# Kernel optimization log

Hardware: AMD Instinct MI355X
Metric: run time of the kernel (lower is better)

## Reference

```python
import jax, jax.numpy as jnp
import numpy as np

SIZE = 11
SIGMA = 1.5
K1, K2, L = 0.01, 0.03, 1.0
C1 = (K1 * L) ** 2
C2 = (K2 * L) ** 2


def _fspecial_gauss(size=SIZE, sigma=SIGMA):
    # mimic MATLAB fspecial('gaussian'): grid -5..5 for size=11
    x, y = np.mgrid[-size // 2 + 1:size // 2 + 1, -size // 2 + 1:size // 2 + 1]
    g = np.exp(-((x.astype(np.float32) ** 2 + y.astype(np.float32) ** 2) / (2.0 * sigma ** 2)))
    g = g / g.sum()
    return jnp.asarray(g, dtype=jnp.float32)[None, None]  # [1,1,11,11] OIHW


def _conv_valid(x, w):
    # x: [B,1,H,W], w: [1,1,k,k], stride 1, no padding
    return jax.lax.conv_general_dilated(
        x, w, window_strides=(1, 1), padding='VALID',
        dimension_numbers=('NCHW', 'OIHW', 'NCHW'))


def setup_inputs() -> dict:
    key = jax.random.key(0)
    k1, k2 = jax.random.split(key)
    sr_image = jax.random.uniform(k1, (16, 3, 512, 512), dtype=jnp.float32)
    hr_image = jax.random.uniform(k2, (16, 3, 512, 512), dtype=jnp.float32)
    return {"sr_image": sr_image, "hr_image": hr_image}


def reference(sr_image, hr_image):
    hr = hr_image[:, 0:1, :, :]
    sr = sr_image[:, 0:1, :, :]
    window = _fspecial_gauss()
    mu1 = _conv_valid(hr, window)
    mu2 = _conv_valid(sr, window)
    mu1_sq = mu1 * mu1
    mu2_sq = mu2 * mu2
    mu1_mu2 = mu1 * mu2
    sigma1_sq = _conv_valid(hr * hr, window) - mu1_sq
    sigma2_sq = _conv_valid(sr * sr, window) - mu2_sq
    sigma12 = _conv_valid(hr * sr, window) - mu1_mu2
    value = ((2 * mu1_mu2 + C1) * (2 * sigma12 + C2)
             / ((mu1_sq + mu2_sq + C1) * (sigma1_sq + sigma2_sq + C2)))
    return jnp.mean(value)
```

## Files before the change

kernel.cpp:

```cpp
#include <hip/hip_runtime.h>
#include <math.h>

#define TW 32
#define TH 32
#define HR 42
#define IMG_W 512
#define OUT_W 502
#define CH_STRIDE (3 * IMG_W * IMG_W)
#define NBLK 4096

__global__ __launch_bounds__(256) void ssim_main_kernel(
    const float* __restrict__ sr_img,
    const float* __restrict__ hr_img,
    float* __restrict__ partial)
{
    __shared__ float hf[5][HR][TW];
    __shared__ float red[4];

    const int t  = threadIdx.x;
    const int x0 = blockIdx.x * TW;
    const int y0 = blockIdx.y * TH;
    const int b  = blockIdx.z;

    float w[11];
    {
        float s = 0.f;
#pragma unroll
        for (int i = 0; i < 11; ++i) {
            float d = (float)(i - 5);
            w[i] = expf(-d * d / 4.5f);
            s += w[i];
        }
        float inv = 1.f / s;
#pragma unroll
        for (int i = 0; i < 11; ++i) w[i] *= inv;
    }

    const float* __restrict__ hrp = hr_img + (size_t)b * CH_STRIDE;
    const float* __restrict__ srp = sr_img + (size_t)b * CH_STRIDE;

    if (t < 168) {
        int r  = t >> 2;
        int c0 = (t & 3) * 8;
        int gy = y0 + r; if (gy > IMG_W - 1) gy = IMG_W - 1;
        const float4* hrow = (const float4*)(hrp + (size_t)gy * IMG_W + x0 + c0);
        const float4* srow = (const float4*)(srp + (size_t)gy * IMG_W + x0 + c0);

        float h[20], s[20];
#pragma unroll
        for (int q = 0; q < 5; ++q) {
            float4 va = hrow[q];
            h[4*q] = va.x; h[4*q+1] = va.y; h[4*q+2] = va.z; h[4*q+3] = va.w;
            float4 vb = srow[q];
            s[4*q] = vb.x; s[4*q+1] = vb.y; s[4*q+2] = vb.z; s[4*q+3] = vb.w;
        }

        float m1[8], m2[8], x2[8], y2[8], xy[8];
#pragma unroll
        for (int j = 0; j < 8; ++j) { m1[j]=0.f; m2[j]=0.f; x2[j]=0.f; y2[j]=0.f; xy[j]=0.f; }
#pragma unroll
        for (int k = 0; k < 11; ++k) {
            float wk = w[k];
#pragma unroll
            for (int j = 0; j < 8; ++j) {
                float a = h[j + k], bb = s[j + k];
                float u = wk * a, v = wk * bb;
                m1[j] += u;      m2[j] += v;
                x2[j] += u * a;  y2[j] += v * bb;  xy[j] += u * bb;
            }
        }
        *(float4*)&hf[0][r][c0]   = make_float4(m1[0],m1[1],m1[2],m1[3]);
        *(float4*)&hf[0][r][c0+4] = make_float4(m1[4],m1[5],m1[6],m1[7]);
        *(float4*)&hf[1][r][c0]   = make_float4(m2[0],m2[1],m2[2],m2[3]);
        *(float4*)&hf[1][r][c0+4] = make_float4(m2[4],m2[5],m2[6],m2[7]);
        *(float4*)&hf[2][r][c0]   = make_float4(x2[0],x2[1],x2[2],x2[3]);
        *(float4*)&hf[2][r][c0+4] = make_float4(x2[4],x2[5],x2[6],x2[7]);
        *(float4*)&hf[3][r][c0]   = make_float4(y2[0],y2[1],y2[2],y2[3]);
        *(float4*)&hf[3][r][c0+4] = make_float4(y2[4],y2[5],y2[6],y2[7]);
        *(float4*)&hf[4][r][c0]   = make_float4(xy[0],xy[1],xy[2],xy[3]);
        *(float4*)&hf[4][r][c0+4] = make_float4(xy[4],xy[5],xy[6],xy[7]);
    }
    __syncthreads();

    const float C1 = 1e-4f, C2 = 9e-4f;
    float local = 0.f;
    if (t < 128) {
        int c  = t & 31;
        int r0 = (t >> 5) * 8;

        float am1[8], am2[8], ax2[8], ay2[8], axy[8];
#pragma unroll
        for (int j = 0; j < 8; ++j) { am1[j]=0.f; am2[j]=0.f; ax2[j]=0.f; ay2[j]=0.f; axy[j]=0.f; }

#pragma unroll
        for (int i = 0; i < 18; ++i) {
            float vm1 = hf[0][r0 + i][c];
            float vm2 = hf[1][r0 + i][c];
            float vx2 = hf[2][r0 + i][c];
            float vy2 = hf[3][r0 + i][c];
            float vxy = hf[4][r0 + i][c];
#pragma unroll
            for (int j = 0; j < 8; ++j) {
                int k = i - j;
                if (k >= 0 && k <= 10) {
                    float wk = w[k];
                    am1[j] += wk * vm1;  am2[j] += wk * vm2;
                    ax2[j] += wk * vx2;  ay2[j] += wk * vy2;
                    axy[j] += wk * vxy;
                }
            }
        }

        int ox = x0 + c;
#pragma unroll
        for (int j = 0; j < 8; ++j) {
            int oy = y0 + r0 + j;
            if (oy < OUT_W && ox < OUT_W) {
                float m1 = am1[j], m2 = am2[j];
                float mu1s = m1 * m1, mu2s = m2 * m2, m12 = m1 * m2;
                float s1 = ax2[j] - mu1s, s2 = ay2[j] - mu2s, s12 = axy[j] - m12;
                float num = (2.f * m12 + C1) * (2.f * s12 + C2);
                float den = (mu1s + mu2s + C1) * (s1 + s2 + C2);
                local += num / den;
            }
        }
    }

#pragma unroll
    for (int off = 32; off > 0; off >>= 1)
        local += __shfl_down(local, off);
    if ((t & 63) == 0) red[t >> 6] = local;
    __syncthreads();
    if (t == 0) {
        int blk = (blockIdx.z * gridDim.y + blockIdx.y) * gridDim.x + blockIdx.x;
        partial[blk] = red[0] + red[1] + red[2] + red[3];
    }
}

__global__ __launch_bounds__(256) void ssim_finalize(
    const float* __restrict__ partial, float* __restrict__ out)
{
    __shared__ float red[4];
    int t = threadIdx.x;
    float s = 0.f;
#pragma unroll
    for (int i = 0; i < NBLK / 256; ++i)
        s += partial[t + i * 256];
#pragma unroll
    for (int off = 32; off > 0; off >>= 1)
        s += __shfl_down(s, off);
    if ((t & 63) == 0) red[t >> 6] = s;
    __syncthreads();
    if (t == 0)
        out[0] = (red[0] + red[1] + red[2] + red[3]) * (1.0f / (16.0f * 502.0f * 502.0f));
}

extern "C" void kernel_launch(void* const* d_in, const int* in_sizes, int n_in,
                              void* d_out, int out_size, void* d_ws, size_t ws_size,
                              hipStream_t stream)
{
    const float* sr = (const float*)d_in[0];
    const float* hr = (const float*)d_in[1];
    float* out = (float*)d_out;
    float* partial = (float*)d_ws;

    dim3 grid(16, 16, 16);
    ssim_main_kernel<<<grid, 256, 0, stream>>>(sr, hr, partial);
    ssim_finalize<<<1, 256, 0, stream>>>(partial, out);
}
```

Measured before the change: 128.9 us.

## Double tile height and replace finalize kernel with atomic accumulation

Raises the tile height from 32 to 64 rows, so each block computes horizontal sums for 74 halo rows in a strided loop and all 256 threads take part in the vertical pass. This shrinks the relative halo overhead (74/64 instead of 42/32) and halves the block count. The separate finalize kernel is removed: each block atomically adds its scaled partial sum to the output, which is zeroed with a memset first. The trade-off is fewer blocks in flight, an atomic float order that is not deterministic, and an extra memset call.

Result: slower. 134.2 us (+4.1%).

```diff
diff --git a/kernel.cpp b/kernel.cpp
--- a/kernel.cpp
+++ b/kernel.cpp
@@ -2,19 +2,19 @@
 #include <math.h>
 
 #define TW 32
-#define TH 32
-#define HR 42
+#define TH 64
+#define HR2 (TH + 10)
+#define NTASK (HR2 * 4)
 #define IMG_W 512
 #define OUT_W 502
 #define CH_STRIDE (3 * IMG_W * IMG_W)
-#define NBLK 4096
 
 __global__ __launch_bounds__(256) void ssim_main_kernel(
     const float* __restrict__ sr_img,
     const float* __restrict__ hr_img,
-    float* __restrict__ partial)
+    float* __restrict__ out)
 {
-    __shared__ float hf[5][HR][TW];
+    __shared__ float hf[5][HR2][TW];
     __shared__ float red[4];
 
     const int t  = threadIdx.x;
@@ -39,9 +39,9 @@
     const float* __restrict__ hrp = hr_img + (size_t)b * CH_STRIDE;
     const float* __restrict__ srp = sr_img + (size_t)b * CH_STRIDE;
 
-    if (t < 168) {
-        int r  = t >> 2;
-        int c0 = (t & 3) * 8;
+    for (int task = t; task < NTASK; task += 256) {
+        int r  = task >> 2;
+        int c0 = (task & 3) * 8;
         int gy = y0 + r; if (gy > IMG_W - 1) gy = IMG_W - 1;
         const float4* hrow = (const float4*)(hrp + (size_t)gy * IMG_W + x0 + c0);
         const float4* srow = (const float4*)(srp + (size_t)gy * IMG_W + x0 + c0);
@@ -84,7 +84,7 @@
 
     const float C1 = 1e-4f, C2 = 9e-4f;
     float local = 0.f;
-    if (t < 128) {
+    {
         int c  = t & 31;
         int r0 = (t >> 5) * 8;
 
@@ -132,27 +132,9 @@
     if ((t & 63) == 0) red[t >> 6] = local;
     __syncthreads();
     if (t == 0) {
-        int blk = (blockIdx.z * gridDim.y + blockIdx.y) * gridDim.x + blockIdx.x;
-        partial[blk] = red[0] + red[1] + red[2] + red[3];
+        float blocksum = red[0] + red[1] + red[2] + red[3];
+        atomicAdd(out, blocksum * (1.0f / (16.0f * 502.0f * 502.0f)));
     }
-}
-
-__global__ __launch_bounds__(256) void ssim_finalize(
-    const float* __restrict__ partial, float* __restrict__ out)
-{
-    __shared__ float red[4];
-    int t = threadIdx.x;
-    float s = 0.f;
-#pragma unroll
-    for (int i = 0; i < NBLK / 256; ++i)
-        s += partial[t + i * 256];
-#pragma unroll
-    for (int off = 32; off > 0; off >>= 1)
-        s += __shfl_down(s, off);
-    if ((t & 63) == 0) red[t >> 6] = s;
-    __syncthreads();
-    if (t == 0)
-        out[0] = (red[0] + red[1] + red[2] + red[3]) * (1.0f / (16.0f * 502.0f * 502.0f));
 }
 
 extern "C" void kernel_launch(void* const* d_in, const int* in_sizes, int n_in,
@@ -162,9 +144,9 @@
     const float* sr = (const float*)d_in[0];
     const float* hr = (const float*)d_in[1];
     float* out = (float*)d_out;
-    float* partial = (float*)d_ws;
 
-    dim3 grid(16, 16, 16);
-    ssim_main_kernel<<<grid, 256, 0, stream>>>(sr, hr, partial);
-    ssim_finalize<<<1, 256, 0, stream>>>(partial, out);
+    hipMemsetAsync(out, 0, sizeof(float), stream);
+
+    dim3 grid(16, 8, 16);
+    ssim_main_kernel<<<grid, 256, 0, stream>>>(sr, hr, out);
 }
```
